# Performance work log

Hardware: AMD Instinct MI355X
Metric: run time of the kernel (lower is better)

The kernel has to match this reference:

```python
import jax, jax.numpy as jnp
import numpy as np

# --- static architecture constants (from tokenizer / module defaults) ---
SIZES = np.array([5, 15, 5] + [34] * 16)
STOPS = np.cumsum(SIZES)                    # seq_stop_position
N_ALLELE = 16
SEG_LEN = 5 + 15 + 5 + 34                   # 59: nflank+peptide+cflank+one mhc
D_MODEL = 256                               # node_feat_size
K_CAND = 8                                  # binding-core candidates per (allele,sample) graph
VOCAB = 30
NEG_FILL = -1000.0


def sinusoidal_pe(length, dim):
    pos = jnp.arange(length, dtype=jnp.float32)[:, None]
    div = jnp.exp(jnp.arange(0, dim, 2, dtype=jnp.float32) * (-jnp.log(10000.0) / dim))
    pe = jnp.zeros((length, dim), dtype=jnp.float32)
    pe = pe.at[:, 0::2].set(jnp.sin(pos * div))
    pe = pe.at[:, 1::2].set(jnp.cos(pos * div))
    return pe


def setup_inputs() -> dict:
    key = jax.random.key(0)
    k1, k2, k3, k4, k5 = jax.random.split(key, 5)
    B = 512
    L = int(STOPS[-1])  # 569
    x_data = jax.random.randint(k1, (B, L), 0, VOCAB, dtype=jnp.int64)
    emb = jax.random.normal(k2, (VOCAB, D_MODEL), dtype=jnp.float32) * 0.02
    emb = emb.at[0].set(0.0)  # padding_idx=0
    # surrogate graph-scorer params (stand-in for DGL AttentiveFP GNN+readout+predict)
    W_pool = jax.random.normal(k3, (K_CAND, SEG_LEN), dtype=jnp.float32) * 0.1
    W_pred = jax.random.normal(k4, (D_MODEL,), dtype=jnp.float32) * 0.05
    b_pred = jax.random.normal(k5, (), dtype=jnp.float32) * 0.01
    return {"x_data": x_data, "emb": emb, "W_pool": W_pool, "W_pred": W_pred, "b_pred": b_pred}


def reference(x_data, emb, W_pool, W_pred, b_pred):
    B = x_data.shape[0]
    G = N_ALLELE * B
    # --- slice into segments (static stop positions) ---
    common = x_data[:, :STOPS[2]]                                     # [B, 25]
    mhc = [x_data[:, STOPS[i + 2]:STOPS[i + 3]] for i in range(N_ALLELE)]
    # feat_full_token: cat over alleles of (common, mhc_i) -> [16B, 59]
    feat_tok = jnp.concatenate(
        [jnp.concatenate([common, m], axis=1) for m in mhc], axis=0)
    mask_full = (feat_tok != 0)                                       # valid positions
    # --- embedding + positional encoding + mask ---
    feat = emb[feat_tok]                                              # [16B, 59, D]
    feat = feat + sinusoidal_pe(SEG_LEN, D_MODEL)[None]               # posenc (eval: no dropout)
    feat = feat * mask_full[..., None].astype(feat.dtype)
    # --- allele presence (first token of each mhc block nonzero) ---
    presence = jnp.concatenate([m[:, 0] != 0 for m in mhc], axis=0)   # [16B]
    # --- surrogate per-candidate graph scores (K candidates per entry) ---
    cand = jnp.einsum('nld,kl->nkd', feat, W_pool)                    # [16B, K, D]
    preds = jnp.einsum('nkd,d->nk', cand, W_pred) + b_pred            # [16B, K]
    # --- segment max / argmax over candidate groups (the torch.unique loop) ---
    # segments are contiguous groups of K; index = repeat(arange(16B), K)
    seg_max = jnp.max(preds, axis=1)                                  # [16B]
    seg_arg = jnp.argmax(preds, axis=1)                               # [16B]
    # --- scatter back into full (allele, sample) grid with fill values ---
    preds_full = jnp.where(presence, seg_max, NEG_FILL).reshape(N_ALLELE, B)
    gidx_full = jnp.where(presence, seg_arg, -1).reshape(N_ALLELE, B)
    # eval-mode output: cat along allele dim then transpose -> [B, 32]
    out = jnp.concatenate([preds_full, gidx_full.astype(preds_full.dtype)], axis=0)
    return jnp.transpose(out, (1, 0))
```

## Files before the change

kernel.cpp:

```cpp
#include <hip/hip_runtime.h>

#define BATCH    512
#define L_TOT    569
#define NALLELE  16
#define SEG_LEN  59
#define D_MODEL  256
#define K_CAND   8
#define VOCAB    30
#define COMMON   25
#define NEG_FILL -1000.0f

__global__ __launch_bounds__(256) void mhc_pool_kernel(
    const int*   __restrict__ x,
    const float* __restrict__ emb,
    const float* __restrict__ wpool,
    const float* __restrict__ wpred,
    const float* __restrict__ bpred,
    float*       __restrict__ out)
{
    __shared__ float s_pa[60];
    __shared__ float s_pb[236];
    __shared__ float s_edot[VOCAB];
    __shared__ float s_pedot[SEG_LEN];
    __shared__ float s_combo[60][32];
    __shared__ float s_wpT[60][8];

    const int   t  = threadIdx.x;
    const float c0 = -0.035977892f;

    if (t < 60) {
        const int j = t >> 1, h = t & 1;
        const float4* e = reinterpret_cast<const float4*>(emb + j * D_MODEL + h * 128);
        const float4* w = reinterpret_cast<const float4*>(wpred + h * 128);
        float a0 = 0, a1 = 0, a2 = 0, a3 = 0;
        #pragma unroll 8
        for (int q = 0; q < 32; ++q) {
            const float4 ev = e[q], wv = w[q];
            a0 = fmaf(ev.x, wv.x, a0);
            a1 = fmaf(ev.y, wv.y, a1);
            a2 = fmaf(ev.z, wv.z, a2);
            a3 = fmaf(ev.w, wv.w, a3);
        }
        s_pa[t] = (a0 + a1) + (a2 + a3);
    }
    if (t < 236) {
        const int   j  = t >> 2, q = t & 3;
        const float pos = (float)j;
        const int   p0  = q * 32;
        float       dv  = __expf(c0 * (float)(2 * p0));
        const float r   = __expf(c0 * 2.0f);
        float a0 = 0.0f, a1 = 0.0f;
        #pragma unroll 8
        for (int p = 0; p < 32; ++p) {
            const float2 wv  = reinterpret_cast<const float2*>(wpred)[p0 + p];
            const float  ang = pos * dv;
            a0 = fmaf(__sinf(ang), wv.x, a0);
            a1 = fmaf(__cosf(ang), wv.y, a1);
            dv *= r;
        }
        s_pb[t] = a0 + a1;
    }
    for (int idx = t; idx < K_CAND * SEG_LEN; idx += 256) {
        const int l = idx >> 3, k = idx & 7;
        s_wpT[l][k] = wpool[k * SEG_LEN + l];
    }
    if (t < 8) s_wpT[59][t] = 0.0f;
    __syncthreads();

    if (t < VOCAB) s_edot[t] = s_pa[2 * t] + s_pa[2 * t + 1];
    if (t >= 64 && t < 64 + SEG_LEN) {
        const int l = t - 64;
        s_pedot[l] = (s_pb[4 * l] + s_pb[4 * l + 1]) + (s_pb[4 * l + 2] + s_pb[4 * l + 3]);
    }
    __syncthreads();

    for (int idx = t; idx < 60 * 32; idx += 256) {
        const int l = idx >> 5, v = idx & 31;
        float s = 0.0f;
        if (l < SEG_LEN && v >= 1 && v < VOCAB) s = s_edot[v] + s_pedot[l];
        s_combo[l][v] = s;
    }
    __syncthreads();

    const float bp   = bpred[0];
    const int   g    = blockIdx.x * 256 + t;
    const int   h    = g & 1;
    const int   pair = g >> 1;
    const int   i    = pair & (NALLELE - 1);
    const int   b    = pair >> 4;
    const int   rowbase = b * L_TOT;
    const int   l0   = h * 30;

    float acc[K_CAND] = {0, 0, 0, 0, 0, 0, 0, 0};
    int   tokp = 0;

    #pragma unroll
    for (int q = 0; q < 30; ++q) {
        const int l = l0 + q;
        int addr;
        if (l < COMMON)       addr = rowbase + l;
        else if (l < SEG_LEN) addr = rowbase + 34 * i + l;
        else                  addr = rowbase;
        const int tok = x[addr];
        if (l0 == 0 && q == COMMON) tokp = tok;
        const float  s   = s_combo[l][tok];
        const float4 wlo = *reinterpret_cast<const float4*>(&s_wpT[l][0]);
        const float4 whi = *reinterpret_cast<const float4*>(&s_wpT[l][4]);
        acc[0] = fmaf(wlo.x, s, acc[0]);
        acc[1] = fmaf(wlo.y, s, acc[1]);
        acc[2] = fmaf(wlo.z, s, acc[2]);
        acc[3] = fmaf(wlo.w, s, acc[3]);
        acc[4] = fmaf(whi.x, s, acc[4]);
        acc[5] = fmaf(whi.y, s, acc[5]);
        acc[6] = fmaf(whi.z, s, acc[6]);
        acc[7] = fmaf(whi.w, s, acc[7]);
    }

    #pragma unroll
    for (int k = 0; k < K_CAND; ++k) acc[k] += __shfl_xor(acc[k], 1);

    float bv = acc[0] + bp; int bk = 0;
    #pragma unroll
    for (int k = 1; k < K_CAND; ++k) {
        const float v = acc[k] + bp;
        if (v > bv) { bv = v; bk = k; }
    }

    if (h == 0) {
        const bool pres = (tokp != 0);
        out[b * 32 + i]           = pres ? bv        : NEG_FILL;
        out[b * 32 + NALLELE + i] = pres ? (float)bk : -1.0f;
    }
}

extern "C" void kernel_launch(void* const* d_in, const int* in_sizes, int n_in,
                              void* d_out, int out_size, void* d_ws, size_t ws_size,
                              hipStream_t stream) {
    const int*   x     = (const int*)  d_in[0];
    const float* emb   = (const float*)d_in[1];
    const float* wpool = (const float*)d_in[2];
    const float* wpred = (const float*)d_in[3];
    const float* bpred = (const float*)d_in[4];
    float*       out   = (float*)d_out;

    mhc_pool_kernel<<<64, 256, 0, stream>>>(x, emb, wpool, wpred, bpred, out);
}
```

Measured before the change: 11.92 us.

## Prefetch tokens before table setup and split each graph across four lanes

Token loads from global memory are issued at kernel start into registers, so their latency overlaps with the per-block computation of the embedding and positional dot-product tables. The s_combo table and one barrier are removed; the score is now computed inline as edot[tok]+pedot[l], with the padding mask applied as a tok != 0 check. Each (allele, sample) graph is now handled by four lanes instead of two, reduced with shuffles, and the grid doubles to 128 blocks. The setup reductions also use shuffles instead of shared scratch arrays. In exchange, the per-block table setup is repeated across twice as many blocks and each thread holds more registers for its prefetched tokens.

Result: faster. 10.90 us (-8.5%).

```diff
diff --git a/kernel.cpp b/kernel.cpp
--- a/kernel.cpp
+++ b/kernel.cpp
@@ -18,92 +18,78 @@
     const float* __restrict__ bpred,
     float*       __restrict__ out)
 {
-    __shared__ float s_pa[60];
-    __shared__ float s_pb[236];
     __shared__ float s_edot[VOCAB];
-    __shared__ float s_pedot[SEG_LEN];
-    __shared__ float s_combo[60][32];
+    __shared__ float s_pedot[60];
     __shared__ float s_wpT[60][8];
 
-    const int   t  = threadIdx.x;
+    const int t = threadIdx.x;
+    const int h = t & 3;
+    const int g = blockIdx.x * 64 + (t >> 2);
+    const int i = g & (NALLELE - 1);
+    const int b = g >> 4;
+    const int rowbase = b * L_TOT;
+
+    int toks[15];
+    #pragma unroll
+    for (int q = 0; q < 15; ++q) {
+        const int l = 15 * h + q;
+        const int addr = (l < COMMON) ? (rowbase + l)
+                       : (l < SEG_LEN) ? (rowbase + 34 * i + l)
+                                       : rowbase;
+        toks[q] = x[addr];
+    }
+    const int tok0 = (h == 0) ? x[rowbase + COMMON + 34 * i] : 0;
+
     const float c0 = -0.035977892f;
-
-    if (t < 60) {
-        const int j = t >> 1, h = t & 1;
-        const float4* e = reinterpret_cast<const float4*>(emb + j * D_MODEL + h * 128);
-        const float4* w = reinterpret_cast<const float4*>(wpred + h * 128);
+    if (t < 120) {
+        const int j = t >> 2, q = t & 3;
+        const float4* e = reinterpret_cast<const float4*>(emb + j * D_MODEL + q * 64);
+        const float4* w = reinterpret_cast<const float4*>(wpred + q * 64);
         float a0 = 0, a1 = 0, a2 = 0, a3 = 0;
-        #pragma unroll 8
-        for (int q = 0; q < 32; ++q) {
-            const float4 ev = e[q], wv = w[q];
+        #pragma unroll
+        for (int p = 0; p < 16; ++p) {
+            const float4 ev = e[p], wv = w[p];
             a0 = fmaf(ev.x, wv.x, a0);
             a1 = fmaf(ev.y, wv.y, a1);
             a2 = fmaf(ev.z, wv.z, a2);
             a3 = fmaf(ev.w, wv.w, a3);
         }
-        s_pa[t] = (a0 + a1) + (a2 + a3);
-    }
-    if (t < 236) {
-        const int   j  = t >> 2, q = t & 3;
+        float part = (a0 + a1) + (a2 + a3);
+        part += __shfl_xor(part, 1);
+        part += __shfl_xor(part, 2);
+        if (q == 0) s_edot[j] = part;
+    } else if (t < 238) {
+        const int tt = t - 120;
+        const int j = tt >> 1, q = tt & 1;
         const float pos = (float)j;
-        const int   p0  = q * 32;
-        float       dv  = __expf(c0 * (float)(2 * p0));
+        float       dv  = q ? __expf(c0 * 64.0f) : 1.0f;
         const float r   = __expf(c0 * 2.0f);
         float a0 = 0.0f, a1 = 0.0f;
-        #pragma unroll 8
+        #pragma unroll
         for (int p = 0; p < 32; ++p) {
-            const float2 wv  = reinterpret_cast<const float2*>(wpred)[p0 + p];
+            const float2 wv  = reinterpret_cast<const float2*>(wpred)[32 * q + p];
             const float  ang = pos * dv;
             a0 = fmaf(__sinf(ang), wv.x, a0);
             a1 = fmaf(__cosf(ang), wv.y, a1);
             dv *= r;
         }
-        s_pb[t] = a0 + a1;
+        float part = a0 + a1;
+        part += __shfl_xor(part, 1);
+        if (q == 0) s_pedot[j] = part;
+        if (tt == 116) s_pedot[59] = 0.0f;
     }
-    for (int idx = t; idx < K_CAND * SEG_LEN; idx += 256) {
+    for (int idx = t; idx < 480; idx += 256) {
         const int l = idx >> 3, k = idx & 7;
-        s_wpT[l][k] = wpool[k * SEG_LEN + l];
-    }
-    if (t < 8) s_wpT[59][t] = 0.0f;
-    __syncthreads();
-
-    if (t < VOCAB) s_edot[t] = s_pa[2 * t] + s_pa[2 * t + 1];
-    if (t >= 64 && t < 64 + SEG_LEN) {
-        const int l = t - 64;
-        s_pedot[l] = (s_pb[4 * l] + s_pb[4 * l + 1]) + (s_pb[4 * l + 2] + s_pb[4 * l + 3]);
+        s_wpT[l][k] = (l < SEG_LEN) ? wpool[k * SEG_LEN + l] : 0.0f;
     }
     __syncthreads();
 
-    for (int idx = t; idx < 60 * 32; idx += 256) {
-        const int l = idx >> 5, v = idx & 31;
-        float s = 0.0f;
-        if (l < SEG_LEN && v >= 1 && v < VOCAB) s = s_edot[v] + s_pedot[l];
-        s_combo[l][v] = s;
-    }
-    __syncthreads();
-
-    const float bp   = bpred[0];
-    const int   g    = blockIdx.x * 256 + t;
-    const int   h    = g & 1;
-    const int   pair = g >> 1;
-    const int   i    = pair & (NALLELE - 1);
-    const int   b    = pair >> 4;
-    const int   rowbase = b * L_TOT;
-    const int   l0   = h * 30;
-
     float acc[K_CAND] = {0, 0, 0, 0, 0, 0, 0, 0};
-    int   tokp = 0;
-
     #pragma unroll
-    for (int q = 0; q < 30; ++q) {
-        const int l = l0 + q;
-        int addr;
-        if (l < COMMON)       addr = rowbase + l;
-        else if (l < SEG_LEN) addr = rowbase + 34 * i + l;
-        else                  addr = rowbase;
-        const int tok = x[addr];
-        if (l0 == 0 && q == COMMON) tokp = tok;
-        const float  s   = s_combo[l][tok];
+    for (int q = 0; q < 15; ++q) {
+        const int   l   = 15 * h + q;
+        const int   tok = toks[q];
+        const float s   = (tok != 0) ? (s_edot[tok] + s_pedot[l]) : 0.0f;
         const float4 wlo = *reinterpret_cast<const float4*>(&s_wpT[l][0]);
         const float4 whi = *reinterpret_cast<const float4*>(&s_wpT[l][4]);
         acc[0] = fmaf(wlo.x, s, acc[0]);
@@ -117,19 +103,19 @@
     }
 
     #pragma unroll
-    for (int k = 0; k < K_CAND; ++k) acc[k] += __shfl_xor(acc[k], 1);
-
-    float bv = acc[0] + bp; int bk = 0;
-    #pragma unroll
-    for (int k = 1; k < K_CAND; ++k) {
-        const float v = acc[k] + bp;
-        if (v > bv) { bv = v; bk = k; }
+    for (int k = 0; k < K_CAND; ++k) {
+        acc[k] += __shfl_xor(acc[k], 1);
+        acc[k] += __shfl_xor(acc[k], 2);
     }
 
     if (h == 0) {
-        const bool pres = (tokp != 0);
-        out[b * 32 + i]           = pres ? bv        : NEG_FILL;
-        out[b * 32 + NALLELE + i] = pres ? (float)bk : -1.0f;
+        float bv = acc[0]; int bk = 0;
+        #pragma unroll
+        for (int k = 1; k < K_CAND; ++k)
+            if (acc[k] > bv) { bv = acc[k]; bk = k; }
+        const bool pres = (tok0 != 0);
+        out[b * 32 + i]           = pres ? (bv + bpred[0]) : NEG_FILL;
+        out[b * 32 + NALLELE + i] = pres ? (float)bk       : -1.0f;
     }
 }
 
@@ -143,5 +129,5 @@
     const float* bpred = (const float*)d_in[4];
     float*       out   = (float*)d_out;
 
-    mhc_pool_kernel<<<64, 256, 0, stream>>>(x, emb, wpool, wpred, bpred, out);
+    mhc_pool_kernel<<<128, 256, 0, stream>>>(x, emb, wpool, wpred, bpred, out);
 }
```
